# Kernel optimization log

Measured on AMD Instinct MI355X. Metric: run time of the kernel, lower is better.

The kernel has to match this reference:

```python
import jax, jax.numpy as jnp
import numpy as np

B, S, D_MODEL, N_HEADS, D_K, D_V = 2, 2048, 1024, 16, 64, 64


def setup_inputs() -> dict:
    key = jax.random.key(0)
    ks = jax.random.split(key, 11)
    s_in = 1.0 / np.sqrt(D_MODEL)
    s_out = 1.0 / np.sqrt(N_HEADS * D_V)
    return {
        "Q": jax.random.normal(ks[0], (B, S, D_MODEL), jnp.float32),
        "K": jax.random.normal(ks[1], (B, S, D_MODEL), jnp.float32),
        "V": jax.random.normal(ks[2], (B, S, D_MODEL), jnp.float32),
        # per-head projection weights (stacked over heads), Linear-style: y = x @ W + b
        "Wq": jax.random.uniform(ks[3], (N_HEADS, D_MODEL, D_K), jnp.float32, -s_in, s_in),
        "bq": jax.random.uniform(ks[4], (N_HEADS, D_K), jnp.float32, -s_in, s_in),
        "Wk": jax.random.uniform(ks[5], (N_HEADS, D_MODEL, D_K), jnp.float32, -s_in, s_in),
        "bk": jax.random.uniform(ks[6], (N_HEADS, D_K), jnp.float32, -s_in, s_in),
        "Wv": jax.random.uniform(ks[7], (N_HEADS, D_MODEL, D_V), jnp.float32, -s_in, s_in),
        "bv": jax.random.uniform(ks[8], (N_HEADS, D_V), jnp.float32, -s_in, s_in),
        "Wo": jax.random.uniform(ks[9], (N_HEADS * D_V, D_MODEL), jnp.float32, -s_out, s_out),
        "bo": jax.random.uniform(ks[10], (D_MODEL,), jnp.float32, -s_out, s_out),
    }


def reference(Q, K, V, Wq, bq, Wk, bk, Wv, bv, Wo, bo):
    # Per-head projections, batched over heads: [B,H,S,dk/dv]
    QW = jnp.einsum("bsd,hdk->bhsk", Q, Wq) + bq[None, :, None, :]
    KW = jnp.einsum("bsd,hdk->bhsk", K, Wk) + bk[None, :, None, :]
    VW = jnp.einsum("bsd,hdv->bhsv", V, Wv) + bv[None, :, None, :]
    scores = jnp.einsum("bhsk,bhtk->bhst", QW, KW)  # [B,H,S,S]
    # Faithful to torch source: softmax(scores)/d_k**1/2 == softmax(scores)/(2*d_k)
    attn = jax.nn.softmax(scores, axis=-1) * (1.0 / (2.0 * D_K))
    heads = jnp.einsum("bhst,bhtv->bhsv", attn, VW)  # [B,H,S,dv]
    # concat heads along feature dim -> [B,S,H*dv], then output projection
    concat = heads.transpose(0, 2, 1, 3).reshape(B, S, N_HEADS * D_V)
    return concat @ Wo + bo
```

## Files before the change

kernel.cpp:

```cpp
#include <hip/hip_runtime.h>

#define BB 2
#define SS 2048
#define DM 1024
#define HH 16
#define DK 64
#define LOG2E 1.44269504088896340736f

typedef __attribute__((ext_vector_type(8))) short short8;
typedef __attribute__((ext_vector_type(4))) float f32x4;
typedef __attribute__((ext_vector_type(16))) float f32x16;

#define MFMA16(a, b, c) __builtin_amdgcn_mfma_f32_16x16x32_bf16(a, b, c, 0, 0, 0)
#define MFMA32(a, b, c) __builtin_amdgcn_mfma_f32_32x32x16_bf16(a, b, c, 0, 0, 0)

#if __has_builtin(__builtin_amdgcn_exp2f)
#define EXP2(x) __builtin_amdgcn_exp2f(x)
#else
#define EXP2(x) __expf((x) * 0.6931471805599453f)
#endif

#define WAITV(N) asm volatile("s_waitcnt vmcnt(" #N ")" ::: "memory")
#define BAR() __builtin_amdgcn_s_barrier()

#define FRAG(buf, row, col) \
    (*(const short8*)&buf[(row) * 64 + ((col) ^ (((row) & 7) << 3))])
#define FRAGV(buf, row, col) \
    (*(const short8*)&buf[(row) * 128 + (((((col) >> 3) ^ ((row) & 15))) << 3)])

static __device__ __forceinline__ unsigned short f2bf(float f) {
    unsigned u = __builtin_bit_cast(unsigned, f);
    u += 0x7fffu + ((u >> 16) & 1u);
    return (unsigned short)(u >> 16);
}

static __device__ __forceinline__ void gld16(const void* g, void* l) {
    __builtin_amdgcn_global_load_lds(
        (const __attribute__((address_space(1))) unsigned int*)g,
        (__attribute__((address_space(3))) unsigned int*)l, 16, 0, 0);
}

__global__ __launch_bounds__(256) void prep_kernel(
    const float* __restrict__ Q, const float* __restrict__ K,
    const float* __restrict__ V,
    const float* __restrict__ Wq, const float* __restrict__ Wk,
    const float* __restrict__ Wv, const float* __restrict__ Wo,
    unsigned short* __restrict__ Qb, unsigned short* __restrict__ Kb,
    unsigned short* __restrict__ Vb,
    unsigned short* __restrict__ Wqt, unsigned short* __restrict__ Wkt,
    unsigned short* __restrict__ Wvt, unsigned short* __restrict__ Wot) {
    __shared__ float t[64][65];
    const int bid = blockIdx.x;
    if (bid < 6144) {
        const int m = bid >> 11;
        const int bx = bid & 2047;
        const float* in = m == 0 ? Q : (m == 1 ? K : V);
        unsigned short* out = m == 0 ? Qb : (m == 1 ? Kb : Vb);
        const int i = (bx * 256 + threadIdx.x) * 8;
        float4 a = *(const float4*)(in + i);
        float4 b = *(const float4*)(in + i + 4);
        union { unsigned short u[8]; uint4 v; } x;
        x.u[0] = f2bf(a.x); x.u[1] = f2bf(a.y); x.u[2] = f2bf(a.z); x.u[3] = f2bf(a.w);
        x.u[4] = f2bf(b.x); x.u[5] = f2bf(b.y); x.u[6] = f2bf(b.z); x.u[7] = f2bf(b.w);
        *(uint4*)(out + i) = x.v;
        return;
    }
    const int idx = bid - 6144;
    const int which = idx >> 8;
    const int bx = idx & 255;
    const float* in;
    unsigned short* out;
    int r0, c0, C;
    if (which < 3) {
        in = which == 0 ? Wq : (which == 1 ? Wk : Wv);
        out = which == 0 ? Wqt : (which == 1 ? Wkt : Wvt);
        const int h = bx >> 4;
        r0 = (bx & 15) * 64; c0 = 0; C = DK;
        in += (size_t)h * DM * DK;
        out += (size_t)h * DK * DM;
    } else {
        in = Wo; out = Wot;
        r0 = (bx & 15) * 64; c0 = (bx >> 4) * 64; C = DM;
    }
    const int lr = threadIdx.x & 63, gg = threadIdx.x >> 6;
    #pragma unroll
    for (int p = 0; p < 16; ++p) {
        const int r = p * 4 + gg;
        t[r][lr] = in[(size_t)(r0 + r) * C + c0 + lr];
    }
    __syncthreads();
    #pragma unroll
    for (int p = 0; p < 16; ++p) {
        const int c = p * 4 + gg;
        out[(size_t)(c0 + c) * DM + r0 + lr] = f2bf(t[lr][c]);
    }
}

#define GSTAGE(Ap, Btp, k0, pp)                                              \
    do {                                                                     \
        _Pragma("unroll")                                                    \
        for (int i = 0; i < 4; ++i) {                                        \
            const int idx = tid + i * 256;                                   \
            const int row = idx >> 3;                                        \
            const int cs = ((idx & 7) ^ (row & 7)) * 8;                      \
            gld16(&Ap[(size_t)(r0 + row) * DM + (k0) + cs], &As[pp][idx * 8]); \
            gld16(&Btp[(size_t)(n0 + row) * DM + (k0) + cs], &Bs[pp][idx * 8]); \
        }                                                                    \
    } while (0)

#define GCOMPUTE(pp)                                                         \
    do {                                                                     \
        _Pragma("unroll")                                                    \
        for (int kc = 0; kc < 2; ++kc) {                                     \
            short8 a[4], b[4];                                               \
            _Pragma("unroll")                                                \
            for (int i = 0; i < 4; ++i) {                                    \
                a[i] = FRAG(As[pp], wr + i * 16 + lr, kc * 32 + lg * 8);     \
                b[i] = FRAG(Bs[pp], wc + i * 16 + lr, kc * 32 + lg * 8);     \
            }                                                                \
            __builtin_amdgcn_s_setprio(1);                                   \
            _Pragma("unroll")                                                \
            for (int mi = 0; mi < 4; ++mi)                                   \
                _Pragma("unroll")                                            \
                for (int ni = 0; ni < 4; ++ni)                               \
                    acc[mi][ni] = MFMA16(a[mi], b[ni], acc[mi][ni]);         \
            __builtin_amdgcn_s_setprio(0);                                   \
        }                                                                    \
    } while (0)

#define GEMM_MAIN(Ap, Btp)                                                   \
    GSTAGE(Ap, Btp, 0, 0);                                                   \
    for (int k = 0; k < 14 * 64; k += 128) {                                 \
        GSTAGE(Ap, Btp, k + 64, 1);                                          \
        WAITV(8); BAR();                                                     \
        GCOMPUTE(0);                                                         \
        BAR();                                                               \
        GSTAGE(Ap, Btp, k + 128, 0);                                         \
        WAITV(8); BAR();                                                     \
        GCOMPUTE(1);                                                         \
        BAR();                                                               \
    }                                                                        \
    GSTAGE(Ap, Btp, 15 * 64, 1);                                             \
    WAITV(8); BAR();                                                         \
    GCOMPUTE(0);                                                             \
    BAR();                                                                   \
    WAITV(0); BAR();                                                         \
    GCOMPUTE(1);

__global__ __launch_bounds__(256) void qkv_gemm_kernel(
    const unsigned short* __restrict__ Qb, const unsigned short* __restrict__ Kb,
    const unsigned short* __restrict__ Vb,
    const unsigned short* __restrict__ Wqt, const unsigned short* __restrict__ Wkt,
    const unsigned short* __restrict__ Wvt,
    const float* __restrict__ bq, const float* __restrict__ bk,
    const float* __restrict__ bv,
    unsigned short* __restrict__ QWp, unsigned short* __restrict__ KWp,
    unsigned short* __restrict__ VWt) {
    __shared__ unsigned short As[2][128 * 64];
    __shared__ unsigned short Bs[2][128 * 64];
    const int z = blockIdx.z;
    const unsigned short* A  = z == 0 ? Qb : (z == 1 ? Kb : Vb);
    const unsigned short* Bt = z == 0 ? Wqt : (z == 1 ? Wkt : Wvt);
    const float* bias = z == 0 ? bq : (z == 1 ? bk : bv);
    const int tid = threadIdx.x;
    const int r0 = blockIdx.x * 128, n0 = blockIdx.y * 128;
    const int w = tid >> 6, lane = tid & 63, lr = lane & 15, lg = lane >> 4;
    const int wr = (w >> 1) * 64, wc = (w & 1) * 64;

    const f32x4 zf = {0.f, 0.f, 0.f, 0.f};
    f32x4 acc[4][4];
    #pragma unroll
    for (int mi = 0; mi < 4; ++mi)
        #pragma unroll
        for (int ni = 0; ni < 4; ++ni) acc[mi][ni] = zf;

    GEMM_MAIN(A, Bt);

    const float scale = (z == 0) ? LOG2E : 1.0f;
    #pragma unroll
    for (int ni = 0; ni < 4; ++ni) {
        const int col = n0 + wc + ni * 16 + lr;
        const float bb = bias[col];
        #pragma unroll
        for (int mi = 0; mi < 4; ++mi) {
            const int rbase = r0 + wr + mi * 16 + lg * 4;
            const f32x4 v = acc[mi][ni];
            if (z == 2) {
                const int b = rbase >> 11, s = rbase & (SS - 1);
                const int h = col >> 6, vv = col & 63;
                union { unsigned short u[4]; unsigned long long q; } x;
                #pragma unroll
                for (int j = 0; j < 4; ++j) x.u[j] = f2bf(v[j] + bb);
                *(unsigned long long*)&VWt[((size_t)(b * HH + h) * 64 + vv) * SS + s] = x.q;
            } else {
                unsigned short* C = z == 0 ? QWp : KWp;
                #pragma unroll
                for (int j = 0; j < 4; ++j)
                    C[(size_t)(rbase + j) * DM + col] = f2bf((v[j] + bb) * scale);
            }
        }
    }
}

__global__ __launch_bounds__(256) void outproj_kernel(
    const unsigned short* __restrict__ A, const unsigned short* __restrict__ Bt,
    const float* __restrict__ bias, float* __restrict__ Cout) {
    __shared__ unsigned short As[2][128 * 64];
    __shared__ unsigned short Bs[2][64 * 64];
    const int tid = threadIdx.x;
    const int r0 = blockIdx.x * 128, n0 = blockIdx.y * 64;
    const int w = tid >> 6, lane = tid & 63, lr = lane & 15, lg = lane >> 4;
    const int wr = (w >> 1) * 64, wc = (w & 1) * 32;

    const f32x4 zf = {0.f, 0.f, 0.f, 0.f};
    f32x4 acc[4][2];
    #pragma unroll
    for (int mi = 0; mi < 4; ++mi)
        #pragma unroll
        for (int ni = 0; ni < 2; ++ni) acc[mi][ni] = zf;

#define OSTAGE(k0, pp)                                                       \
    do {                                                                     \
        _Pragma("unroll")                                                    \
        for (int i = 0; i < 4; ++i) {                                        \
            const int idx = tid + i * 256;                                   \
            const int row = idx >> 3;                                        \
            const int cs = ((idx & 7) ^ (row & 7)) * 8;                      \
            gld16(&A[(size_t)(r0 + row) * DM + (k0) + cs], &As[pp][idx * 8]); \
        }                                                                    \
        _Pragma("unroll")                                                    \
        for (int i = 0; i < 2; ++i) {                                        \
            const int idx = tid + i * 256;                                   \
            const int row = idx >> 3;                                        \
            const int cs = ((idx & 7) ^ (row & 7)) * 8;                      \
            gld16(&Bt[(size_t)(n0 + row) * DM + (k0) + cs], &Bs[pp][idx * 8]); \
        }                                                                    \
    } while (0)

#define OCOMP(pp)                                                            \
    do {                                                                     \
        _Pragma("unroll")                                                    \
        for (int kc = 0; kc < 2; ++kc) {                                     \
            short8 a[4], b[2];                                               \
            _Pragma("unroll")                                                \
            for (int i = 0; i < 4; ++i)                                      \
                a[i] = FRAG(As[pp], wr + i * 16 + lr, kc * 32 + lg * 8);     \
            _Pragma("unroll")                                                \
            for (int i = 0; i < 2; ++i)                                      \
                b[i] = FRAG(Bs[pp], wc + i * 16 + lr, kc * 32 + lg * 8);     \
            __builtin_amdgcn_s_setprio(1);                                   \
            _Pragma("unroll")                                                \
            for (int mi = 0; mi < 4; ++mi)                                   \
                _Pragma("unroll")                                            \
                for (int ni = 0; ni < 2; ++ni)                               \
                    acc[mi][ni] = MFMA16(a[mi], b[ni], acc[mi][ni]);         \
            __builtin_amdgcn_s_setprio(0);                                   \
        }                                                                    \
    } while (0)

    OSTAGE(0, 0);
    for (int k = 0; k < 14 * 64; k += 128) {
        OSTAGE(k + 64, 1);
        WAITV(6); BAR();
        OCOMP(0);
        BAR();
        OSTAGE(k + 128, 0);
        WAITV(6); BAR();
        OCOMP(1);
        BAR();
    }
    OSTAGE(15 * 64, 1);
    WAITV(6); BAR();
    OCOMP(0);
    BAR();
    WAITV(0); BAR();
    OCOMP(1);
#undef OSTAGE
#undef OCOMP

    #pragma unroll
    for (int ni = 0; ni < 2; ++ni) {
        const int col = n0 + wc + ni * 16 + lr;
        const float bb = bias[col];
        #pragma unroll
        for (int mi = 0; mi < 4; ++mi) {
            const int rbase = r0 + wr + mi * 16 + lg * 4;
            const f32x4 v = acc[mi][ni];
            #pragma unroll
            for (int j = 0; j < 4; ++j)
                Cout[(size_t)(rbase + j) * DM + col] = v[j] + bb;
        }
    }
}

__global__ __launch_bounds__(256, 2) void attn_kernel(
    const unsigned short* __restrict__ QW,
    const unsigned short* __restrict__ KW,
    const unsigned short* __restrict__ VWt,
    unsigned short* __restrict__ CC) {
    __shared__ unsigned short Ks[2][128 * 64];
    __shared__ unsigned short Vs[2][64 * 128];
    const int tid = threadIdx.x;
    const int w = tid >> 6, lane = tid & 63;
    const int ql = lane & 31, hi = lane >> 5, hi8 = hi * 8;

    const int wgid = blockIdx.x;
    const int kk = wgid >> 3;
    const int bh = (kk >> 4) * 8 + (wgid & 7);
    const int b = bh >> 4, h = bh & 15;
    const int row0 = (kk & 15) * 128;
    const int q = row0 + w * 32 + ql;

    short8 qf[4];
    const unsigned short* Qp = QW + ((size_t)b * SS + q) * DM + h * DK;
    #pragma unroll
    for (int kc = 0; kc < 4; ++kc)
        qf[kc] = *(const short8*)(Qp + kc * 16 + hi8);

    const unsigned short* Kp = KW + (size_t)b * SS * DM + h * DK;
    const unsigned short* Vt = VWt + (size_t)bh * 64 * SS;

#define STAGE(t0, pp)                                                        \
    do {                                                                     \
        _Pragma("unroll")                                                    \
        for (int i = 0; i < 4; ++i) {                                        \
            const int idx = tid + i * 256;                                   \
            const int kr = idx >> 3;                                         \
            const int kc8 = ((idx & 7) ^ (kr & 7)) * 8;                      \
            gld16(&Kp[(size_t)((t0) + kr) * DM + kc8], &Ks[pp][idx * 8]);    \
            const int vr = idx >> 4;                                         \
            const int vc8 = ((idx & 15) ^ (vr & 15)) * 8;                    \
            gld16(&Vt[(size_t)vr * SS + (t0) + vc8], &Vs[pp][idx * 8]);      \
        }                                                                    \
    } while (0)

    const f32x16 z16 = {0.f};
    const short8 ones = {(short)0x3F80, (short)0x3F80, (short)0x3F80, (short)0x3F80,
                         (short)0x3F80, (short)0x3F80, (short)0x3F80, (short)0x3F80};
    f32x16 o0 = z16, o1 = z16, lv = z16;

#define PACK2(sx, pa0, pa1)                                                      \
    do {                                                                         \
        unsigned x, x2, y, y2, u, u2, v, v2;                                     \
        asm("v_cvt_pk_bf16_f32 %0, %1, %2" : "=v"(x)  : "v"(sx[0]), "v"(sx[1])); \
        asm("v_cvt_pk_bf16_f32 %0, %1, %2" : "=v"(x2) : "v"(sx[2]), "v"(sx[3])); \
        asm("v_cvt_pk_bf16_f32 %0, %1, %2" : "=v"(y)  : "v"(sx[4]), "v"(sx[5])); \
        asm("v_cvt_pk_bf16_f32 %0, %1, %2" : "=v"(y2) : "v"(sx[6]), "v"(sx[7])); \
        asm("v_cvt_pk_bf16_f32 %0, %1, %2" : "=v"(u)  : "v"(sx[8]), "v"(sx[9])); \
        asm("v_cvt_pk_bf16_f32 %0, %1, %2" : "=v"(u2) : "v"(sx[10]), "v"(sx[11])); \
        asm("v_cvt_pk_bf16_f32 %0, %1, %2" : "=v"(v)  : "v"(sx[12]), "v"(sx[13])); \
        asm("v_cvt_pk_bf16_f32 %0, %1, %2" : "=v"(v2) : "v"(sx[14]), "v"(sx[15])); \
        asm("v_permlane32_swap_b32 %0, %1" : "+v"(x),  "+v"(y));                 \
        asm("v_permlane32_swap_b32 %0, %1" : "+v"(x2), "+v"(y2));                \
        asm("v_permlane32_swap_b32 %0, %1" : "+v"(u),  "+v"(v));                 \
        asm("v_permlane32_swap_b32 %0, %1" : "+v"(u2), "+v"(v2));                \
        union { unsigned uu[4]; short8 s8; } k0, k1;                             \
        k0.uu[0] = x; k0.uu[1] = x2; k0.uu[2] = y; k0.uu[3] = y2;                \
        k1.uu[0] = u; k1.uu[1] = u2; k1.uu[2] = v; k1.uu[3] = v2;                \
        pa0 = k0.s8; pa1 = k1.s8;                                                \
    } while (0)

#define PVC(pp, sx, c)                                                           \
    do {                                                                         \
        _Pragma("unroll")                                                        \
        for (int r = 0; r < 16; ++r) sx[r] = EXP2(sx[r]);                        \
        short8 pa0, pa1;                                                         \
        PACK2(sx, pa0, pa1);                                                     \
        __builtin_amdgcn_s_setprio(1);                                           \
        o0 = MFMA32(FRAGV(Vs[pp], ql, (c) * 32 + hi8), pa0, o0);                 \
        lv = MFMA32(ones, pa0, lv);                                              \
        o1 = MFMA32(FRAGV(Vs[pp], 32 + ql, (c) * 32 + hi8), pa0, o1);            \
        o0 = MFMA32(FRAGV(Vs[pp], ql, (c) * 32 + 16 + hi8), pa1, o0);            \
        lv = MFMA32(ones, pa1, lv);                                              \
        o1 = MFMA32(FRAGV(Vs[pp], 32 + ql, (c) * 32 + 16 + hi8), pa1, o1);       \
        __builtin_amdgcn_s_setprio(0);                                           \
    } while (0)

#define COMPUTE(pp)                                                              \
    do {                                                                         \
        f32x16 s0, s1, s2, s3;                                                   \
        __builtin_amdgcn_s_setprio(1);                                           \
        s0 = MFMA32(FRAG(Ks[pp], ql, hi8), qf[0], z16);                          \
        s1 = MFMA32(FRAG(Ks[pp], 32 + ql, hi8), qf[0], z16);                     \
        s2 = MFMA32(FRAG(Ks[pp], 64 + ql, hi8), qf[0], z16);                     \
        s3 = MFMA32(FRAG(Ks[pp], 96 + ql, hi8), qf[0], z16);                     \
        _Pragma("unroll")                                                        \
        for (int kc = 1; kc < 4; ++kc) {                                         \
            s0 = MFMA32(FRAG(Ks[pp], ql, kc * 16 + hi8), qf[kc], s0);            \
            s1 = MFMA32(FRAG(Ks[pp], 32 + ql, kc * 16 + hi8), qf[kc], s1);       \
            s2 = MFMA32(FRAG(Ks[pp], 64 + ql, kc * 16 + hi8), qf[kc], s2);       \
            s3 = MFMA32(FRAG(Ks[pp], 96 + ql, kc * 16 + hi8), qf[kc], s3);       \
        }                                                                        \
        __builtin_amdgcn_s_setprio(0);                                           \
        PVC(pp, s0, 0);                                                          \
        PVC(pp, s1, 1);                                                          \
        PVC(pp, s2, 2);                                                          \
        PVC(pp, s3, 3);                                                          \
    } while (0)

    STAGE(0, 0);
    for (int t = 0; t < 14; t += 2) {
        STAGE((t + 1) * 128, 1);
        WAITV(8); BAR();
        COMPUTE(0);
        BAR();
        STAGE((t + 2) * 128, 0);
        WAITV(8); BAR();
        COMPUTE(1);
        BAR();
    }
    STAGE(15 * 128, 1);
    WAITV(8); BAR();
    COMPUTE(0);
    BAR();
    WAITV(0); BAR();
    COMPUTE(1);
#undef STAGE
#undef COMPUTE
#undef PVC

    const float inv = 1.0f / (lv[0] * 128.0f);
    unsigned short* cp = CC + ((size_t)b * SS + q) * DM + h * DK;
    #pragma unroll
    for (int vt = 0; vt < 2; ++vt) {
        const f32x16 ov = vt ? o1 : o0;
        #pragma unroll
        for (int m2 = 0; m2 < 4; ++m2) {
            union { unsigned short u[4]; unsigned long long q8; } pk;
            #pragma unroll
            for (int c = 0; c < 4; ++c) pk.u[c] = f2bf(ov[m2 * 4 + c] * inv);
            *(unsigned long long*)(cp + vt * 32 + m2 * 8 + hi * 4) = pk.q8;
        }
    }
}

extern "C" void kernel_launch(void* const* d_in, const int* in_sizes, int n_in,
                              void* d_out, int out_size, void* d_ws, size_t ws_size,
                              hipStream_t stream) {
    const float* Q  = (const float*)d_in[0];
    const float* K  = (const float*)d_in[1];
    const float* V  = (const float*)d_in[2];
    const float* Wq = (const float*)d_in[3];
    const float* bq = (const float*)d_in[4];
    const float* Wk = (const float*)d_in[5];
    const float* bk = (const float*)d_in[6];
    const float* Wv = (const float*)d_in[7];
    const float* bv = (const float*)d_in[8];
    const float* Wo = (const float*)d_in[9];
    const float* bo = (const float*)d_in[10];
    float* out = (float*)d_out;

    unsigned short* ws = (unsigned short*)d_ws;
    const size_t MK = (size_t)BB * SS * DM;
    const size_t WK = (size_t)DM * DM;
    unsigned short* Qb  = ws;
    unsigned short* Kb  = Qb + MK;
    unsigned short* Vb  = Kb + MK;
    unsigned short* Wqt = Vb + MK;
    unsigned short* Wkt = Wqt + WK;
    unsigned short* Wvt = Wkt + WK;
    unsigned short* Wot = Wvt + WK;
    unsigned short* QWp = Wot + WK;
    unsigned short* KWp = QWp + MK;
    unsigned short* VWt = KWp + MK;
    unsigned short* CCp = Qb;

    dim3 blk(256);
    const int M = BB * SS;

    hipLaunchKernelGGL(prep_kernel, dim3(7168), blk, 0, stream,
                       Q, K, V, Wq, Wk, Wv, Wo,
                       Qb, Kb, Vb, Wqt, Wkt, Wvt, Wot);

    hipLaunchKernelGGL(qkv_gemm_kernel, dim3(M / 128, 8, 3), blk, 0, stream,
                       Qb, Kb, Vb, Wqt, Wkt, Wvt, bq, bk, bv, QWp, KWp, VWt);

    hipLaunchKernelGGL(attn_kernel, dim3(512), blk, 0, stream,
                       QWp, KWp, VWt, CCp);

    hipLaunchKernelGGL(outproj_kernel, dim3(M / 128, DM / 64), blk, 0, stream,
                       CCp, Wot, bo, out);
}
```

Baseline: 117.5 us.

## Use 512-thread blocks with 8 warps in QKV projection GEMM

The QKV projection GEMM keeps its 128x128 tile but now runs 8 waves per block instead of 4. Each wave computes a 64x32 sub-tile, which halves the accumulator registers per wave and halves the global-to-LDS loads per thread. The vmcnt waits are adjusted to match the smaller number of loads in flight. The intent is more waves to hide latency, at the cost of less B-fragment reuse per wave and more barrier participants. The GEMM_MAIN macro is removed; the outproj kernel may have relied on it unless it has its own copy.

Measured after the change: 115.8 us. Within noise of the previous version (-1.4%).

```diff
diff --git a/kernel.cpp b/kernel.cpp
--- a/kernel.cpp
+++ b/kernel.cpp
@@ -96,11 +96,11 @@
     }
 }
 
-#define GSTAGE(Ap, Btp, k0, pp)                                              \
+#define QSTAGE(Ap, Btp, k0, pp)                                              \
     do {                                                                     \
         _Pragma("unroll")                                                    \
-        for (int i = 0; i < 4; ++i) {                                        \
-            const int idx = tid + i * 256;                                   \
+        for (int i = 0; i < 2; ++i) {                                        \
+            const int idx = tid + i * 512;                                   \
             const int row = idx >> 3;                                        \
             const int cs = ((idx & 7) ^ (row & 7)) * 8;                      \
             gld16(&Ap[(size_t)(r0 + row) * DM + (k0) + cs], &As[pp][idx * 8]); \
@@ -108,46 +108,28 @@
         }                                                                    \
     } while (0)
 
-#define GCOMPUTE(pp)                                                         \
+#define QCOMP(pp)                                                            \
     do {                                                                     \
         _Pragma("unroll")                                                    \
         for (int kc = 0; kc < 2; ++kc) {                                     \
-            short8 a[4], b[4];                                               \
-            _Pragma("unroll")                                                \
-            for (int i = 0; i < 4; ++i) {                                    \
+            short8 a[4], b[2];                                               \
+            _Pragma("unroll")                                                \
+            for (int i = 0; i < 4; ++i)                                      \
                 a[i] = FRAG(As[pp], wr + i * 16 + lr, kc * 32 + lg * 8);     \
+            _Pragma("unroll")                                                \
+            for (int i = 0; i < 2; ++i)                                      \
                 b[i] = FRAG(Bs[pp], wc + i * 16 + lr, kc * 32 + lg * 8);     \
-            }                                                                \
             __builtin_amdgcn_s_setprio(1);                                   \
             _Pragma("unroll")                                                \
             for (int mi = 0; mi < 4; ++mi)                                   \
                 _Pragma("unroll")                                            \
-                for (int ni = 0; ni < 4; ++ni)                               \
+                for (int ni = 0; ni < 2; ++ni)                               \
                     acc[mi][ni] = MFMA16(a[mi], b[ni], acc[mi][ni]);         \
             __builtin_amdgcn_s_setprio(0);                                   \
         }                                                                    \
     } while (0)
 
-#define GEMM_MAIN(Ap, Btp)                                                   \
-    GSTAGE(Ap, Btp, 0, 0);                                                   \
-    for (int k = 0; k < 14 * 64; k += 128) {                                 \
-        GSTAGE(Ap, Btp, k + 64, 1);                                          \
-        WAITV(8); BAR();                                                     \
-        GCOMPUTE(0);                                                         \
-        BAR();                                                               \
-        GSTAGE(Ap, Btp, k + 128, 0);                                         \
-        WAITV(8); BAR();                                                     \
-        GCOMPUTE(1);                                                         \
-        BAR();                                                               \
-    }                                                                        \
-    GSTAGE(Ap, Btp, 15 * 64, 1);                                             \
-    WAITV(8); BAR();                                                         \
-    GCOMPUTE(0);                                                             \
-    BAR();                                                                   \
-    WAITV(0); BAR();                                                         \
-    GCOMPUTE(1);
-
-__global__ __launch_bounds__(256) void qkv_gemm_kernel(
+__global__ __launch_bounds__(512) void qkv_gemm_kernel(
     const unsigned short* __restrict__ Qb, const unsigned short* __restrict__ Kb,
     const unsigned short* __restrict__ Vb,
     const unsigned short* __restrict__ Wqt, const unsigned short* __restrict__ Wkt,
@@ -165,20 +147,36 @@
     const int tid = threadIdx.x;
     const int r0 = blockIdx.x * 128, n0 = blockIdx.y * 128;
     const int w = tid >> 6, lane = tid & 63, lr = lane & 15, lg = lane >> 4;
-    const int wr = (w >> 1) * 64, wc = (w & 1) * 64;
+    const int wr = (w >> 2) * 64, wc = (w & 3) * 32;
 
     const f32x4 zf = {0.f, 0.f, 0.f, 0.f};
-    f32x4 acc[4][4];
+    f32x4 acc[4][2];
     #pragma unroll
     for (int mi = 0; mi < 4; ++mi)
         #pragma unroll
-        for (int ni = 0; ni < 4; ++ni) acc[mi][ni] = zf;
-
-    GEMM_MAIN(A, Bt);
+        for (int ni = 0; ni < 2; ++ni) acc[mi][ni] = zf;
+
+    QSTAGE(A, Bt, 0, 0);
+    for (int k = 0; k < 14 * 64; k += 128) {
+        QSTAGE(A, Bt, k + 64, 1);
+        WAITV(4); BAR();
+        QCOMP(0);
+        BAR();
+        QSTAGE(A, Bt, k + 128, 0);
+        WAITV(4); BAR();
+        QCOMP(1);
+        BAR();
+    }
+    QSTAGE(A, Bt, 15 * 64, 1);
+    WAITV(4); BAR();
+    QCOMP(0);
+    BAR();
+    WAITV(0); BAR();
+    QCOMP(1);
 
     const float scale = (z == 0) ? LOG2E : 1.0f;
     #pragma unroll
-    for (int ni = 0; ni < 4; ++ni) {
+    for (int ni = 0; ni < 2; ++ni) {
         const int col = n0 + wc + ni * 16 + lr;
         const float bb = bias[col];
         #pragma unroll
@@ -472,7 +470,7 @@
                        Q, K, V, Wq, Wk, Wv, Wo,
                        Qb, Kb, Vb, Wqt, Wkt, Wvt, Wot);
 
-    hipLaunchKernelGGL(qkv_gemm_kernel, dim3(M / 128, 8, 3), blk, 0, stream,
+    hipLaunchKernelGGL(qkv_gemm_kernel, dim3(M / 128, 8, 3), dim3(512), 0, stream,
                        Qb, Kb, Vb, Wqt, Wkt, Wvt, bq, bk, bv, QWp, KWp, VWt);
 
     hipLaunchKernelGGL(attn_kernel, dim3(512), blk, 0, stream,
```
